# Performance work log

Hardware: AMD Instinct MI355X
Metric: run time of the kernel (lower is better)

The kernel has to match this reference:

```python
import jax, jax.numpy as jnp
from jax import lax
import numpy as np

B, T, H, W, CIN, F, NC = 8, 16, 32, 32, 6, 64, 10
BN_EPS = 1e-3


def _conv(x, k):
    # x: [B,H,W,Cin], k: [3,3,Cin,Cout], SAME padding
    return lax.conv_general_dilated(x, k, (1, 1), 'SAME',
                                    dimension_numbers=('NHWC', 'HWIO', 'NHWC'))


def _hard_sigmoid(x):
    return jnp.clip(0.2 * x + 0.5, 0.0, 1.0)


def _convlstm(x_seq, Wx, Wh, b):
    # x_seq: [B,T,H,W,Cin] -> [B,T,H,W,F]; keras gate order [i,f,c,o]
    nb, nt, nh, nw, _ = x_seq.shape
    nf = Wh.shape[2]
    h0 = jnp.zeros((nb, nh, nw, nf), x_seq.dtype)

    def step(carry, xt):
        h, c = carry
        z = _conv(xt, Wx) + _conv(h, Wh) + b
        i, f, g, o = jnp.split(z, 4, axis=-1)
        i, f, o = _hard_sigmoid(i), _hard_sigmoid(f), _hard_sigmoid(o)
        c = f * c + i * jnp.tanh(g)
        h = o * jnp.tanh(c)
        return (h, c), h

    _, hs = lax.scan(step, (h0, h0), jnp.moveaxis(x_seq, 1, 0))  # scan over T
    return jnp.moveaxis(hs, 0, 1)


def _bn(x, gamma, beta, mean, var):
    # inference-mode BatchNorm over channel axis, eps=1e-3 (keras default)
    inv = gamma * lax.rsqrt(var + BN_EPS)
    return (x - mean) * inv + beta


def setup_inputs() -> dict:
    key = jax.random.key(0)
    ks = jax.random.split(key, 12)
    s = 0.05
    d = {
        'inputs': jax.random.normal(ks[0], (B, T, H, W, CIN), jnp.float32),
        'l0_Wx': jax.random.normal(ks[1], (3, 3, CIN, 4 * F), jnp.float32) * s,
        'l0_Wh': jax.random.normal(ks[2], (3, 3, F, 4 * F), jnp.float32) * s,
        'l0_b': jnp.zeros((4 * F,), jnp.float32),
        'l0_gamma': jnp.ones((F,), jnp.float32),
        'l0_beta': jnp.zeros((F,), jnp.float32),
        'l0_mean': jnp.zeros((F,), jnp.float32),
        'l0_var': jnp.ones((F,), jnp.float32),
        'l1_Wx': jax.random.normal(ks[3], (3, 3, F, 4 * F), jnp.float32) * s,
        'l1_Wh': jax.random.normal(ks[4], (3, 3, F, 4 * F), jnp.float32) * s,
        'l1_b': jnp.zeros((4 * F,), jnp.float32),
        'l1_gamma': jnp.ones((F,), jnp.float32),
        'l1_beta': jnp.zeros((F,), jnp.float32),
        'l1_mean': jnp.zeros((F,), jnp.float32),
        'l1_var': jnp.ones((F,), jnp.float32),
        'dense_W': jax.random.normal(ks[5], (F, NC), jnp.float32) * s,
        'dense_b': jnp.zeros((NC,), jnp.float32),
    }
    return d


def reference(inputs, l0_Wx, l0_Wh, l0_b, l0_gamma, l0_beta, l0_mean, l0_var,
              l1_Wx, l1_Wh, l1_b, l1_gamma, l1_beta, l1_mean, l1_var,
              dense_W, dense_b):
    x = _convlstm(inputs, l0_Wx, l0_Wh, l0_b)
    x = _bn(x, l0_gamma, l0_beta, l0_mean, l0_var)
    x = _convlstm(x, l1_Wx, l1_Wh, l1_b)
    x = _bn(x, l1_gamma, l1_beta, l1_mean, l1_var)
    x = jax.nn.softmax(jnp.einsum('bthwf,fc->bthwc', x, dense_W) + dense_b, axis=-1)
    return jnp.mean(x, axis=(1, 2, 3))  # GlobalAveragePooling3D -> [B, NC]
```

## Files before the change

### kernel.cpp

```cpp
#include <hip/hip_runtime.h>
#include <math.h>

typedef __attribute__((ext_vector_type(8))) short short8v;
typedef __attribute__((ext_vector_type(4))) float float4v;

constexpr int Bsz = 8, Tn = 16, CINc = 6, Fc = 64, NCc = 10;
constexpr int PIX = 8192;
constexpr float BN_EPS = 1e-3f;

constexpr int FR_L0X = 0;
constexpr int FR_L0H = 16384;
constexpr int FR_L1X = 163840;
constexpr int FR_L1H = 311296;
constexpr int FR_TOTAL = 458752;

__device__ __forceinline__ ushort f2bf(float f) {
    union { float f; unsigned u; } v; v.f = f;
    unsigned r = v.u + 0x7FFFu + ((v.u >> 16) & 1u);
    return (ushort)(r >> 16);
}
__device__ __forceinline__ float bf2f(ushort u) {
    union { unsigned u; float f; } v; v.u = ((unsigned)u) << 16; return v.f;
}
__device__ __forceinline__ float hsig(float x) {
    return fminf(fmaxf(0.2f * x + 0.5f, 0.0f), 1.0f);
}

#define GLDS(srcp, dstp) \
    __builtin_amdgcn_global_load_lds((const __attribute__((address_space(1))) void*)(srcp), \
                                     (__attribute__((address_space(3))) void*)(dstp), 16, 0, 0)

__global__ __launch_bounds__(256) void prep_x(const float* __restrict__ in,
                                              ushort* __restrict__ xb) {
    int o = blockIdx.x * 256 + threadIdx.x;
    if (o >= Tn * PIX * CINc) return;
    int t = o / (PIX * CINc);
    int rem = o - t * (PIX * CINc);
    int pix = rem / CINc, c = rem - pix * CINc;
    int b = pix >> 10, p = pix & 1023;
    xb[o] = f2bf(in[((b * Tn + t) * 1024 + p) * CINc + c]);
}

__global__ __launch_bounds__(256) void prep_w(const float* __restrict__ W0x,
                                              const float* __restrict__ W0h,
                                              const float* __restrict__ W1x,
                                              const float* __restrict__ W1h,
                                              ushort* __restrict__ F) {
    int o = blockIdx.x * 256 + threadIdx.x;
    if (o >= FR_TOTAL) return;
    const float* W; int K; int base;
    if (o < FR_L0H)      { W = W0x; K = 54;  base = FR_L0X; }
    else if (o < FR_L1X) { W = W0h; K = 576; base = FR_L0H; }
    else if (o < FR_L1H) { W = W1x; K = 576; base = FR_L1X; }
    else                 { W = W1h; K = 576; base = FR_L1H; }
    int r = o - base;
    int e = r & 7, lane = (r >> 3) & 63, j = (r >> 9) & 7, nh = (r >> 12) & 1, kc = r >> 13;
    int nt = ((j >> 1) << 2) + nh * 2 + (j & 1);
    int k = kc * 32 + ((lane >> 4) * 4) + (e & 3) + 16 * (e >> 2);
    int n = nt * 16 + (lane & 15);
    F[o] = (k < K) ? f2bf(W[k * 256 + n]) : (ushort)0;
}

__global__ __launch_bounds__(640) void prep_dense(
    const float* __restrict__ dW, const float* __restrict__ dB,
    const float* __restrict__ g, const float* __restrict__ be,
    const float* __restrict__ mn, const float* __restrict__ vr,
    float* __restrict__ dWf, float* __restrict__ dBf)
{
    __shared__ float sc[64], sh[64];
    int tid = threadIdx.x;
    if (tid < 64) {
        float s = g[tid] * rsqrtf(vr[tid] + BN_EPS);
        sc[tid] = s; sh[tid] = be[tid] - mn[tid] * s;
    }
    __syncthreads();
    if (tid < 640) { int f = tid / 10; dWf[tid] = sc[f] * dW[tid]; }
    if (tid < NCc) {
        float a = dB[tid];
        for (int f = 0; f < 64; ++f) a += sh[f] * dW[f * 10 + tid];
        dBf[tid] = a;
    }
}

__global__ __launch_bounds__(256) void init_zero(float* c0, float* c1,
                                                 ushort* h0, ushort* h1,
                                                 ushort* h0b, ushort* h1b, float* out) {
    int i = blockIdx.x * 256 + threadIdx.x;
    if (i < PIX * Fc) { c0[i] = 0.f; c1[i] = 0.f; h0[i] = 0; h1[i] = 0; h0b[i] = 0; h1b[i] = 0; }
    if (i < Bsz * NCc) out[i] = 0.f;
}

__global__ __launch_bounds__(256, 3) void step_tri(
    int t,
    const ushort* __restrict__ Xb,
    const ushort* __restrict__ Bf0X, const ushort* __restrict__ Bf0H,
    const float* __restrict__ b0,
    float* __restrict__ C0, const ushort* __restrict__ H0prev, ushort* __restrict__ H0cur,
    ushort* __restrict__ X1s,
    const float* __restrict__ g0, const float* __restrict__ be0,
    const float* __restrict__ mn0, const float* __restrict__ v0,
    const ushort* __restrict__ Bf1X, const ushort* __restrict__ Bf1H,
    const float* __restrict__ b1, float* __restrict__ Z1,
    float* __restrict__ C1, const ushort* __restrict__ H1prev, ushort* __restrict__ H1cur,
    ushort* __restrict__ H1s)
{
    const int grp = blockIdx.x >> 8;
    int s;
    if (grp == 0)      { s = t;     if (s >= Tn) return; }
    else if (grp == 1) { s = t - 1; if (s < 0 || s >= Tn) return; }
    else               { s = t - 2; if (s < 0 || s >= Tn) return; }

    __shared__ ushort As[64 * 72];
    __shared__ ushort Bs[2][8192];

    const int tid = threadIdx.x;
    const int wid = tid >> 6, lane = tid & 63;
    const int wm = wid >> 1, wn = wid & 1;
    const int bid = blockIdx.x & 255;
    const int bm = bid >> 1, nh = bid & 1;
    const int m0 = bm * 64;

    const int p_local = tid >> 2, kq = tid & 3;
    const int p_global = m0 + p_local;
    const int img = p_global >> 10, pp = p_global & 1023;
    const int py = pp >> 5, px = pp & 31;

    const int ar0 = (wm * 32 + 0  + (lane & 15)) * 144 + (lane >> 4) * 8;
    const int ar1 = (wm * 32 + 16 + (lane & 15)) * 144 + (lane >> 4) * 8;
    const int awr = p_local * 144 + kq * 16;

    const ushort* __restrict__ Xt   = Xb + s * PIX * CINc;
    const ushort* __restrict__ X1t  = X1s + (size_t)s * (PIX * Fc);
    float* __restrict__ Zp = Z1 + (((size_t)s * 128 + bm) * 2 + nh) * 8192;
    const int TOT = (grp == 0) ? 10 : 9;

    auto stageB = [&](int q, int buf) {
        const ushort *g0p, *g1p;
        if (grp == 0) {
            if (q == 0) { g0p = Bf0X + (nh << 12); g1p = Bf0X + ((2 + nh) << 12); }
            else { int tp = q - 1;
                   g0p = Bf0H + ((4 * tp + nh) << 12);
                   g1p = Bf0H + ((4 * tp + 2 + nh) << 12); }
        } else if (grp == 1) {
            g0p = Bf1X + ((4 * q + nh) << 12);
            g1p = Bf1X + ((4 * q + 2 + nh) << 12);
        } else {
            g0p = Bf1H + ((4 * q + nh) << 12);
            g1p = Bf1H + ((4 * q + 2 + nh) << 12);
        }
        ushort* d = &Bs[buf][0];
        GLDS(g0p + (tid << 3),         d + wid * 512);
        GLDS(g0p + ((256 + tid) << 3), d + 2048 + wid * 512);
        GLDS(g1p + (tid << 3),         d + 4096 + wid * 512);
        GLDS(g1p + ((256 + tid) << 3), d + 4096 + 2048 + wid * 512);
    };
    auto gather64 = [&](const ushort* __restrict__ P, int tap, uint4& a0, uint4& a1) {
        a0 = make_uint4(0u, 0u, 0u, 0u); a1 = a0;
        int dy = tap / 3 - 1, dx = tap % 3 - 1;
        int gy = py + dy, gx = px + dx;
        if ((unsigned)gy < 32u && (unsigned)gx < 32u) {
            const ushort* bp = P + (((img << 10) + gy * 32 + gx) << 6) + (kq << 3);
            a0 = *(const uint4*)bp;
            a1 = *(const uint4*)(bp + 32);
        }
    };
    auto gatherA = [&](int q, uint4& a0, uint4& a1) {
        if (grp == 0) {
            if (q == 0) {
                union { ushort s[8]; uint4 u; } p0, p1;
#pragma unroll
                for (int j = 0; j < 8; ++j) {
                    {
                        int kg = kq * 8 + j;
                        int tap = kg / 6, c = kg - tap * 6;
                        int dy = tap / 3 - 1, dx = tap % 3 - 1;
                        int gy = py + dy, gx = px + dx;
                        ushort v = 0;
                        if ((unsigned)gy < 32u && (unsigned)gx < 32u)
                            v = Xt[((img << 10) + gy * 32 + gx) * 6 + c];
                        p0.s[j] = v;
                    }
                    {
                        int kg = 32 + kq * 8 + j;
                        ushort v = 0;
                        if (kg < 54) {
                            int tap = kg / 6, c = kg - tap * 6;
                            int dy = tap / 3 - 1, dx = tap % 3 - 1;
                            int gy = py + dy, gx = px + dx;
                            if ((unsigned)gy < 32u && (unsigned)gx < 32u)
                                v = Xt[((img << 10) + gy * 32 + gx) * 6 + c];
                        }
                        p1.s[j] = v;
                    }
                }
                a0 = p0.u; a1 = p1.u;
                return;
            }
            gather64(H0prev, q - 1, a0, a1);
        } else if (grp == 1) {
            gather64(X1t, q, a0, a1);
        } else {
            gather64(H1prev, q, a0, a1);
        }
    };

    float4v acc[8];
    if (grp == 2) {
#pragma unroll
        for (int a = 0; a < 8; ++a)
            acc[a] = *(const float4v*)(Zp + (((wid * 8 + a) * 64 + lane) << 2));
    } else {
        const float* __restrict__ bias = (grp == 0) ? b0 : b1;
        const int hch = (nh * 2 + wn) * 16 + (lane & 15);
#pragma unroll
        for (int g = 0; g < 4; ++g) {
            const float bb = bias[g * 64 + hch];
#pragma unroll
            for (int r = 0; r < 4; ++r) { acc[g * 2 + 0][r] = bb; acc[g * 2 + 1][r] = bb; }
        }
    }

    uint4 av0, av1;
    gatherA(0, av0, av1);
    stageB(0, 0);

    for (int q = 0; q < TOT; ++q) {
        __syncthreads();
        *(uint4*)((char*)As + awr) = av0;
        *(uint4*)((char*)As + awr + 64) = av1;
        __syncthreads();

        union { struct { uint2 lo, hi; } u; short8v s; } a00, a10, a01, a11;
        const char* base = (const char*)As;
        a00.u.lo = *(const uint2*)(base + ar0);      a00.u.hi = *(const uint2*)(base + ar0 + 32);
        a10.u.lo = *(const uint2*)(base + ar1);      a10.u.hi = *(const uint2*)(base + ar1 + 32);
        a01.u.lo = *(const uint2*)(base + ar0 + 64); a01.u.hi = *(const uint2*)(base + ar0 + 96);
        a11.u.lo = *(const uint2*)(base + ar1 + 64); a11.u.hi = *(const uint2*)(base + ar1 + 96);

        const ushort* bs = &Bs[q & 1][0];
        union { uint4 u; short8v s; } b0r[4], b1r[4];
#pragma unroll
        for (int g = 0; g < 4; ++g) {
            const int j = g * 2 + wn;
            b0r[g].u = *(const uint4*)(bs + ((j * 64 + lane) << 3));
            b1r[g].u = *(const uint4*)(bs + 4096 + ((j * 64 + lane) << 3));
        }

        if (q + 1 < TOT) {
            stageB(q + 1, (q + 1) & 1);
            gatherA(q + 1, av0, av1);
        }

#pragma unroll
        for (int g = 0; g < 4; ++g) {
            acc[g * 2 + 0] = __builtin_amdgcn_mfma_f32_16x16x32_bf16(a00.s, b0r[g].s, acc[g * 2 + 0], 0, 0, 0);
            acc[g * 2 + 1] = __builtin_amdgcn_mfma_f32_16x16x32_bf16(a10.s, b0r[g].s, acc[g * 2 + 1], 0, 0, 0);
        }
#pragma unroll
        for (int g = 0; g < 4; ++g) {
            acc[g * 2 + 0] = __builtin_amdgcn_mfma_f32_16x16x32_bf16(a01.s, b1r[g].s, acc[g * 2 + 0], 0, 0, 0);
            acc[g * 2 + 1] = __builtin_amdgcn_mfma_f32_16x16x32_bf16(a11.s, b1r[g].s, acc[g * 2 + 1], 0, 0, 0);
        }
    }

    if (grp == 1) {
#pragma unroll
        for (int a = 0; a < 8; ++a) {
            float4 o;
            o.x = acc[a][0]; o.y = acc[a][1]; o.z = acc[a][2]; o.w = acc[a][3];
            *(float4*)(Zp + (((wid * 8 + a) * 64 + lane) << 2)) = o;
        }
        return;
    }

    float* __restrict__ C  = (grp == 0) ? C0 : C1;
    ushort* __restrict__ Hc = (grp == 0) ? H0cur : H1cur;
    ushort* __restrict__ Seq = (grp == 0) ? (X1s + (size_t)s * (PIX * Fc))
                                          : (H1s + (size_t)s * (PIX * Fc));
    const int ch = (nh * 2 + wn) * 16 + (lane & 15);
    float inv = 0.f, mu = 0.f, bet = 0.f;
    if (grp == 0) {
        inv = g0[ch] * rsqrtf(v0[ch] + BN_EPS);
        mu = mn0[ch]; bet = be0[ch];
    }
#pragma unroll
    for (int mf = 0; mf < 2; ++mf) {
#pragma unroll
        for (int r = 0; r < 4; ++r) {
            const int p = m0 + wm * 32 + mf * 16 + (lane >> 4) * 4 + r;
            const int o = p * 64 + ch;
            float zi = acc[0 + mf][r];
            float zf = acc[2 + mf][r];
            float zg = acc[4 + mf][r];
            float zo = acc[6 + mf][r];
            float cv = hsig(zf) * C[o] + hsig(zi) * tanhf(zg);
            C[o] = cv;
            float h = hsig(zo) * tanhf(cv);
            Hc[o] = f2bf(h);
            Seq[o] = (grp == 0) ? f2bf((h - mu) * inv + bet) : f2bf(h);
        }
    }
}

__global__ __launch_bounds__(256) void pool_all(
    const ushort* __restrict__ H1seq, const float* __restrict__ dWf,
    const float* __restrict__ dBf, float* __restrict__ out)
{
    __shared__ float wlds[640];
    __shared__ float accs[NCc];
    const int tid = threadIdx.x;
    for (int i = tid; i < 640; i += 256) wlds[i] = dWf[i];
    if (tid < NCc) accs[tid] = 0.f;
    __syncthreads();

    const int gid = blockIdx.x * 256 + tid;
    const int b = (gid & 8191) >> 10;

    float logit[NCc];
#pragma unroll
    for (int c = 0; c < NCc; ++c) logit[c] = dBf[c];
    const ushort* hp = H1seq + (size_t)gid * Fc;
#pragma unroll
    for (int f0 = 0; f0 < 8; ++f0) {
        union { uint4 u; ushort s[8]; } hu;
        hu.u = *(const uint4*)(hp + f0 * 8);
#pragma unroll
        for (int j = 0; j < 8; ++j) {
            float v = bf2f(hu.s[j]);
            const float* w = &wlds[(f0 * 8 + j) * 10];
#pragma unroll
            for (int c = 0; c < NCc; ++c) logit[c] += v * w[c];
        }
    }
    float mx = logit[0];
#pragma unroll
    for (int c = 1; c < NCc; ++c) mx = fmaxf(mx, logit[c]);
    float p[NCc]; float ssum = 0.f;
#pragma unroll
    for (int c = 0; c < NCc; ++c) { p[c] = expf(logit[c] - mx); ssum += p[c]; }
    float invs = 1.f / ssum;

#pragma unroll
    for (int c = 0; c < NCc; ++c) {
        float v = p[c] * invs;
        v += __shfl_xor(v, 1);
        v += __shfl_xor(v, 2);
        v += __shfl_xor(v, 4);
        v += __shfl_xor(v, 8);
        v += __shfl_xor(v, 16);
        v += __shfl_xor(v, 32);
        if ((tid & 63) == 0) atomicAdd(&accs[c], v);
    }
    __syncthreads();
    if (tid < NCc)
        atomicAdd(&out[b * NCc + tid], accs[tid] * (1.0f / 16384.0f));
}

extern "C" void kernel_launch(void* const* d_in, const int* in_sizes, int n_in,
                              void* d_out, int out_size, void* d_ws, size_t ws_size,
                              hipStream_t stream) {
    const float* in    = (const float*)d_in[0];
    const float* l0Wx  = (const float*)d_in[1];
    const float* l0Wh  = (const float*)d_in[2];
    const float* l0b   = (const float*)d_in[3];
    const float* l0g   = (const float*)d_in[4];
    const float* l0be  = (const float*)d_in[5];
    const float* l0m   = (const float*)d_in[6];
    const float* l0v   = (const float*)d_in[7];
    const float* l1Wx  = (const float*)d_in[8];
    const float* l1Wh  = (const float*)d_in[9];
    const float* l1b   = (const float*)d_in[10];
    const float* l1g   = (const float*)d_in[11];
    const float* l1be  = (const float*)d_in[12];
    const float* l1m   = (const float*)d_in[13];
    const float* l1v   = (const float*)d_in[14];
    const float* dW    = (const float*)d_in[15];
    const float* dB    = (const float*)d_in[16];
    float* out = (float*)d_out;

    float* ws   = (float*)d_ws;
    float* c0   = ws;
    float* c1   = c0 + 524288;
    float* z1   = c1 + 524288;
    ushort* us  = (ushort*)(z1 + 33554432);
    ushort* h0p0 = us;
    ushort* h0p1 = h0p0 + 524288;
    ushort* h1p0 = h0p1 + 524288;
    ushort* h1p1 = h1p0 + 524288;
    ushort* xb  = h1p1 + 524288;
    ushort* x1  = xb + 786432;
    ushort* h1s = x1 + 8388608;
    ushort* wf  = h1s + 8388608;
    float* dWf  = (float*)(wf + 458752);
    float* dBf  = dWf + 640;

    ushort* h0p[2] = { h0p0, h0p1 };
    ushort* h1p[2] = { h1p0, h1p1 };

    prep_x<<<3072, 256, 0, stream>>>(in, xb);
    prep_w<<<1792, 256, 0, stream>>>(l0Wx, l0Wh, l1Wx, l1Wh, wf);
    prep_dense<<<1, 640, 0, stream>>>(dW, dB, l1g, l1be, l1m, l1v, dWf, dBf);
    init_zero<<<2048, 256, 0, stream>>>(c0, c1, h0p0, h1p0, h0p1, h1p1, out);

    for (int t = 0; t < Tn + 2; ++t) {
        step_tri<<<768, 256, 0, stream>>>(
            t, xb,
            wf + FR_L0X, wf + FR_L0H, l0b,
            c0, h0p[t & 1], h0p[(t + 1) & 1], x1,
            l0g, l0be, l0m, l0v,
            wf + FR_L1X, wf + FR_L1H, l1b, z1,
            c1, h1p[t & 1], h1p[(t + 1) & 1], h1s);
    }
    pool_all<<<512, 256, 0, stream>>>(h1s, dWf, dBf, out);
}
```

Before: 373.7 us.

## Stage halo tile of inputs in LDS once instead of per-tap gathers

Instead of gathering the im2col A operand from global memory for each of the 9 conv taps and writing it into a small LDS buffer every iteration, each block loads a 2-row halo tile (4x34 pixels x 64 channels, plus a 6-channel x tile for layer 0) into LDS once. MFMA A fragments are then read directly from the halo tile with per-tap offsets. This cuts redundant global loads (each pixel was fetched up to 9 times) and removes one of the two barriers per iteration. The cost is more LDS use, an upfront load that is not overlapped, and scalar LDS gathers for the layer-0 input fragment.

New measurement: 330.7 us. 11.5% less time.

```diff
diff --git a/kernel.cpp b/kernel.cpp
--- a/kernel.cpp
+++ b/kernel.cpp
@@ -110,7 +110,8 @@
     else if (grp == 1) { s = t - 1; if (s < 0 || s >= Tn) return; }
     else               { s = t - 2; if (s < 0 || s >= Tn) return; }
 
-    __shared__ ushort As[64 * 72];
+    __shared__ ushort Hh[136 * 68];
+    __shared__ ushort Xh[136 * 8];
     __shared__ ushort Bs[2][8192];
 
     const int tid = threadIdx.x;
@@ -119,20 +120,14 @@
     const int bid = blockIdx.x & 255;
     const int bm = bid >> 1, nh = bid & 1;
     const int m0 = bm * 64;
-
-    const int p_local = tid >> 2, kq = tid & 3;
-    const int p_global = m0 + p_local;
-    const int img = p_global >> 10, pp = p_global & 1023;
-    const int py = pp >> 5, px = pp & 31;
-
-    const int ar0 = (wm * 32 + 0  + (lane & 15)) * 144 + (lane >> 4) * 8;
-    const int ar1 = (wm * 32 + 16 + (lane & 15)) * 144 + (lane >> 4) * 8;
-    const int awr = p_local * 144 + kq * 16;
+    const int img = m0 >> 10;
+    const int py0 = (m0 & 1023) >> 5;
 
     const ushort* __restrict__ Xt   = Xb + s * PIX * CINc;
     const ushort* __restrict__ X1t  = X1s + (size_t)s * (PIX * Fc);
     float* __restrict__ Zp = Z1 + (((size_t)s * 128 + bm) * 2 + nh) * 8192;
     const int TOT = (grp == 0) ? 10 : 9;
+    const ushort* __restrict__ Psrc = (grp == 0) ? H0prev : (grp == 1 ? X1t : H1prev);
 
     auto stageB = [&](int q, int buf) {
         const ushort *g0p, *g1p;
@@ -154,55 +149,38 @@
         GLDS(g1p + (tid << 3),         d + 4096 + wid * 512);
         GLDS(g1p + ((256 + tid) << 3), d + 4096 + 2048 + wid * 512);
     };
-    auto gather64 = [&](const ushort* __restrict__ P, int tap, uint4& a0, uint4& a1) {
-        a0 = make_uint4(0u, 0u, 0u, 0u); a1 = a0;
-        int dy = tap / 3 - 1, dx = tap % 3 - 1;
-        int gy = py + dy, gx = px + dx;
-        if ((unsigned)gy < 32u && (unsigned)gx < 32u) {
-            const ushort* bp = P + (((img << 10) + gy * 32 + gx) << 6) + (kq << 3);
-            a0 = *(const uint4*)bp;
-            a1 = *(const uint4*)(bp + 32);
-        }
-    };
-    auto gatherA = [&](int q, uint4& a0, uint4& a1) {
-        if (grp == 0) {
-            if (q == 0) {
-                union { ushort s[8]; uint4 u; } p0, p1;
-#pragma unroll
-                for (int j = 0; j < 8; ++j) {
-                    {
-                        int kg = kq * 8 + j;
-                        int tap = kg / 6, c = kg - tap * 6;
-                        int dy = tap / 3 - 1, dx = tap % 3 - 1;
-                        int gy = py + dy, gx = px + dx;
-                        ushort v = 0;
-                        if ((unsigned)gy < 32u && (unsigned)gx < 32u)
-                            v = Xt[((img << 10) + gy * 32 + gx) * 6 + c];
-                        p0.s[j] = v;
-                    }
-                    {
-                        int kg = 32 + kq * 8 + j;
-                        ushort v = 0;
-                        if (kg < 54) {
-                            int tap = kg / 6, c = kg - tap * 6;
-                            int dy = tap / 3 - 1, dx = tap % 3 - 1;
-                            int gy = py + dy, gx = px + dx;
-                            if ((unsigned)gy < 32u && (unsigned)gx < 32u)
-                                v = Xt[((img << 10) + gy * 32 + gx) * 6 + c];
-                        }
-                        p1.s[j] = v;
-                    }
-                }
-                a0 = p0.u; a1 = p1.u;
-                return;
+
+    stageB(0, 0);
+#pragma unroll
+    for (int u = 0; u < 5; ++u) {
+        int idx = tid + u * 256;
+        if (idx < 1088) {
+            int slot = idx >> 3, part = idx & 7;
+            int yy = slot / 34, xx = slot - yy * 34;
+            int gy = py0 - 1 + yy, gx = xx - 1;
+            uint4 v = make_uint4(0u, 0u, 0u, 0u);
+            if ((unsigned)gy < 32u && (unsigned)gx < 32u)
+                v = *(const uint4*)(Psrc + (((img << 10) + gy * 32 + gx) << 6) + part * 8);
+            ushort* d = &Hh[slot * 68 + part * 8];
+            *(uint2*)(d)     = make_uint2(v.x, v.y);
+            *(uint2*)(d + 4) = make_uint2(v.z, v.w);
+        }
+    }
+    if (grp == 0) {
+#pragma unroll
+        for (int u = 0; u < 4; ++u) {
+            int idx = tid + u * 256;
+            if (idx < 816) {
+                int slot = idx / 6, c = idx - slot * 6;
+                int yy = slot / 34, xx = slot - yy * 34;
+                int gy = py0 - 1 + yy, gx = xx - 1;
+                ushort v = 0;
+                if ((unsigned)gy < 32u && (unsigned)gx < 32u)
+                    v = Xt[((img << 10) + gy * 32 + gx) * 6 + c];
+                Xh[slot * 8 + c] = v;
             }
-            gather64(H0prev, q - 1, a0, a1);
-        } else if (grp == 1) {
-            gather64(X1t, q, a0, a1);
-        } else {
-            gather64(H1prev, q, a0, a1);
-        }
-    };
+        }
+    }
 
     float4v acc[8];
     if (grp == 2) {
@@ -220,22 +198,47 @@
         }
     }
 
-    uint4 av0, av1;
-    gatherA(0, av0, av1);
-    stageB(0, 0);
+    const int p0x = wm * 32 + (lane & 15);
+    const int p1x = p0x + 16;
+    const int y0r = p0x >> 5, x0c = p0x & 31;
+    const int y1r = p1x >> 5, x1c = p1x & 31;
+    const int coff = (lane >> 4) << 2;
+
+    auto xfrag = [&](int lry, int lcx, int half) -> short8v {
+        union { ushort e[8]; short8v v; } r;
+#pragma unroll
+        for (int e = 0; e < 8; ++e) {
+            int kg = half * 32 + coff + (e & 3) + 16 * (e >> 2);
+            ushort val = 0;
+            if (kg < 54) {
+                int tap = kg / 6, c = kg - tap * 6;
+                int dy = tap / 3 - 1, dxx = tap % 3 - 1;
+                val = Xh[((lry + dy + 1) * 34 + (lcx + dxx + 1)) * 8 + c];
+            }
+            r.e[e] = val;
+        }
+        return r.v;
+    };
+
+    __syncthreads();
 
     for (int q = 0; q < TOT; ++q) {
-        __syncthreads();
-        *(uint4*)((char*)As + awr) = av0;
-        *(uint4*)((char*)As + awr + 64) = av1;
-        __syncthreads();
+        if (q + 1 < TOT) stageB(q + 1, (q + 1) & 1);
 
         union { struct { uint2 lo, hi; } u; short8v s; } a00, a10, a01, a11;
-        const char* base = (const char*)As;
-        a00.u.lo = *(const uint2*)(base + ar0);      a00.u.hi = *(const uint2*)(base + ar0 + 32);
-        a10.u.lo = *(const uint2*)(base + ar1);      a10.u.hi = *(const uint2*)(base + ar1 + 32);
-        a01.u.lo = *(const uint2*)(base + ar0 + 64); a01.u.hi = *(const uint2*)(base + ar0 + 96);
-        a11.u.lo = *(const uint2*)(base + ar1 + 64); a11.u.hi = *(const uint2*)(base + ar1 + 96);
+        if (grp == 0 && q == 0) {
+            a00.s = xfrag(y0r, x0c, 0); a01.s = xfrag(y0r, x0c, 1);
+            a10.s = xfrag(y1r, x1c, 0); a11.s = xfrag(y1r, x1c, 1);
+        } else {
+            const int tap = (grp == 0) ? q - 1 : q;
+            const int dy = tap / 3 - 1, dxx = tap % 3 - 1;
+            const ushort* h0r = &Hh[((y0r + dy + 1) * 34 + (x0c + dxx + 1)) * 68 + coff];
+            const ushort* h1r = &Hh[((y1r + dy + 1) * 34 + (x1c + dxx + 1)) * 68 + coff];
+            a00.u.lo = *(const uint2*)(h0r);      a00.u.hi = *(const uint2*)(h0r + 16);
+            a01.u.lo = *(const uint2*)(h0r + 32); a01.u.hi = *(const uint2*)(h0r + 48);
+            a10.u.lo = *(const uint2*)(h1r);      a10.u.hi = *(const uint2*)(h1r + 16);
+            a11.u.lo = *(const uint2*)(h1r + 32); a11.u.hi = *(const uint2*)(h1r + 48);
+        }
 
         const ushort* bs = &Bs[q & 1][0];
         union { uint4 u; short8v s; } b0r[4], b1r[4];
@@ -246,11 +249,6 @@
             b1r[g].u = *(const uint4*)(bs + 4096 + ((j * 64 + lane) << 3));
         }
 
-        if (q + 1 < TOT) {
-            stageB(q + 1, (q + 1) & 1);
-            gatherA(q + 1, av0, av1);
-        }
-
 #pragma unroll
         for (int g = 0; g < 4; ++g) {
             acc[g * 2 + 0] = __builtin_amdgcn_mfma_f32_16x16x32_bf16(a00.s, b0r[g].s, acc[g * 2 + 0], 0, 0, 0);
@@ -261,6 +259,8 @@
             acc[g * 2 + 0] = __builtin_amdgcn_mfma_f32_16x16x32_bf16(a01.s, b1r[g].s, acc[g * 2 + 0], 0, 0, 0);
             acc[g * 2 + 1] = __builtin_amdgcn_mfma_f32_16x16x32_bf16(a11.s, b1r[g].s, acc[g * 2 + 1], 0, 0, 0);
         }
+
+        __syncthreads();
     }
 
     if (grp == 1) {
```
